# Performance work log

Hardware: AMD Instinct MI355X
Metric: run time of the kernel (lower is better)

Reference implementation:

```python
import jax, jax.numpy as jnp
from jax import lax
import numpy as np

# Mamba mixer dims (mamba-1.4b scale)
D_MODEL, D_INNER, D_STATE, D_CONV, DT_RANK = 2048, 4096, 16, 4, 128
B, L = 2, 1024


def setup_inputs() -> dict:
    key = jax.random.key(0)
    ks = jax.random.split(key, 10)
    s = 0.02
    x = jax.random.normal(ks[0], (B, L, D_MODEL), jnp.float32)
    W_in = jax.random.normal(ks[1], (2 * D_INNER, D_MODEL), jnp.float32) * s
    conv_w = jax.random.normal(ks[2], (D_INNER, D_CONV), jnp.float32) * s  # depthwise kernel
    conv_b = jax.random.normal(ks[3], (D_INNER,), jnp.float32) * s
    W_x = jax.random.normal(ks[4], (DT_RANK + 2 * D_STATE, D_INNER), jnp.float32) * s
    W_dt = jax.random.normal(ks[5], (D_INNER, DT_RANK), jnp.float32) * s
    b_dt = jax.random.normal(ks[6], (D_INNER,), jnp.float32) * s
    # S4D-real init: A = -[1..d_state] per channel
    A_log = jnp.log(jnp.broadcast_to(jnp.arange(1, D_STATE + 1, dtype=jnp.float32), (D_INNER, D_STATE)))
    Dp = jnp.ones((D_INNER,), jnp.float32)
    W_out = jax.random.normal(ks[7], (D_MODEL, D_INNER), jnp.float32) * s
    return {"x": x, "W_in": W_in, "conv_w": conv_w, "conv_b": conv_b,
            "W_x": W_x, "W_dt": W_dt, "b_dt": b_dt, "A_log": A_log,
            "Dp": Dp, "W_out": W_out}


def reference(x, W_in, conv_w, conv_b, W_x, W_dt, b_dt, A_log, Dp, W_out):
    b, l, _ = x.shape
    d_inner, d_state = A_log.shape
    dt_rank = W_dt.shape[1]
    d_conv = conv_w.shape[1]

    # in_proj -> x branch and gate z   [b,l,2*d_inner]
    xz = jnp.einsum('bld,ed->ble', x, W_in)
    xp, z = jnp.split(xz, 2, axis=-1)

    # causal depthwise conv1d (kernel size d_conv) + SiLU
    xpad = jnp.pad(xp, ((0, 0), (d_conv - 1, 0), (0, 0)))
    xc = conv_b + sum(xpad[:, k:k + l, :] * conv_w[:, k] for k in range(d_conv))
    xc = jax.nn.silu(xc)

    # input-dependent dt, B, C
    dbc = jnp.einsum('ble,fe->blf', xc, W_x)
    dt = dbc[..., :dt_rank]
    Bm = dbc[..., dt_rank:dt_rank + d_state]          # [b,l,s]
    Cm = dbc[..., dt_rank + d_state:]                 # [b,l,s]
    delta = jax.nn.softplus(jnp.einsum('blr,er->ble', dt, W_dt) + b_dt)  # [b,l,e]

    A = -jnp.exp(A_log)                               # [e,s]
    dA = jnp.exp(delta[..., None] * A)                # [b,l,e,s]
    dBx = delta[..., None] * Bm[:, :, None, :] * xc[..., None]  # [b,l,e,s]

    def step(h, inp):
        dA_t, dBx_t = inp                             # [b,e,s]
        h = dA_t * h + dBx_t
        return h, h

    h0 = jnp.zeros((b, d_inner, d_state), x.dtype)
    _, hs = lax.scan(step, h0, (jnp.swapaxes(dA, 0, 1), jnp.swapaxes(dBx, 0, 1)))
    hs = jnp.swapaxes(hs, 0, 1)                       # [b,l,e,s]

    y = jnp.einsum('bles,bls->ble', hs, Cm) + xc * Dp
    y = y * jax.nn.silu(z)
    return jnp.einsum('ble,de->bld', y, W_out)
```

## Files before the change

### kernel.cpp

```cpp
#include <hip/hip_runtime.h>
#include <cstdint>


typedef __bf16 bf16x8 __attribute__((ext_vector_type(8)));
typedef float f32x4 __attribute__((ext_vector_type(4)));

__device__ __forceinline__ unsigned short f2bf(float f) {
  uint32_t u = __float_as_uint(f);
  u += 0x7FFFu + ((u >> 16) & 1u);
  return (unsigned short)(u >> 16);
}

__device__ __forceinline__ float bf2f(unsigned short v) {
  return __uint_as_float(((uint32_t)v) << 16);
}

__device__ __forceinline__ float silu_f(float v) {
  return v / (1.f + __expf(-v));
}

__device__ __forceinline__ float softplus_f(float v) {
  return (v > 20.f) ? v : log1pf(__expf(v));
}

__global__ void cast_all(const float* __restrict__ x, const float* __restrict__ W_in,
                         const float* __restrict__ W_out, const float* __restrict__ W_dt,
                         const float* __restrict__ W_x,
                         unsigned short* __restrict__ x_bf, unsigned short* __restrict__ Win_bf,
                         unsigned short* __restrict__ Wout_bf, unsigned short* __restrict__ Wdt_bf,
                         unsigned short* __restrict__ Wx_bf) {
  int i = blockIdx.x * 256 + threadIdx.x;
  const float4* s4; ushort4* d4; int j;
  if (i < 1048576)      { s4 = (const float4*)x;     d4 = (ushort4*)x_bf;    j = i; }
  else if (i < 5242880) { s4 = (const float4*)W_in;  d4 = (ushort4*)Win_bf;  j = i - 1048576; }
  else if (i < 7340032) { s4 = (const float4*)W_out; d4 = (ushort4*)Wout_bf; j = i - 5242880; }
  else if (i < 7471104) { s4 = (const float4*)W_dt;  d4 = (ushort4*)Wdt_bf;  j = i - 7340032; }
  else {
    j = i - 7471104;
    ushort4 o = {0, 0, 0, 0};
    if (j < 163840) {
      float4 v = ((const float4*)W_x)[j];
      o.x = f2bf(v.x); o.y = f2bf(v.y); o.z = f2bf(v.z); o.w = f2bf(v.w);
    }
    ((ushort4*)Wx_bf)[j] = o;
    return;
  }
  float4 v = s4[j];
  ushort4 o; o.x = f2bf(v.x); o.y = f2bf(v.y); o.z = f2bf(v.z); o.w = f2bf(v.w);
  d4[j] = o;
}

#define BM 128
#define BN 128
#define BKK 32

__device__ __forceinline__ void stage_tile(const unsigned short* __restrict__ G,
                                           int ldK, int g0, int k0,
                                           unsigned short* lds, int wave, int lane) {
#pragma unroll
  for (int c = 0; c < 2; ++c) {
    int row = c * 64 + wave * 16 + (lane >> 2);
    int col = (lane & 3) * 8;
    const unsigned short* src = G + (size_t)(g0 + row) * ldK + (k0 + col);
    unsigned short* dst = lds + c * 2048 + wave * 512;
    __builtin_amdgcn_global_load_lds((__attribute__((address_space(1))) void*)(src),
                                     (__attribute__((address_space(3))) void*)(dst),
                                     16, 0, 0);
  }
}

__global__ __launch_bounds__(256)
void gemm_bt(const unsigned short* __restrict__ A, const unsigned short* __restrict__ B,
             float* __restrict__ C, int M, int N, int ldK, int kchunk,
             const float* __restrict__ bias_sp) {
  __shared__ unsigned short As[BM * BKK];
  __shared__ unsigned short Bs[BN * BKK];
  const int tid = threadIdx.x;
  const int wave = tid >> 6, lane = tid & 63;
  const int wr = wave >> 1, wc = wave & 1;
  const int m0 = blockIdx.y * BM, n0 = blockIdx.x * BN;
  const int lr = lane & 15, lg = lane >> 4;
  const int kb = blockIdx.z * kchunk, ke = kb + kchunk;
  C += (size_t)blockIdx.z * M * N;

  f32x4 zero = {0.f, 0.f, 0.f, 0.f};
  f32x4 acc[4][4];
#pragma unroll
  for (int i = 0; i < 4; ++i)
#pragma unroll
    for (int j = 0; j < 4; ++j) acc[i][j] = zero;

  for (int k0 = kb; k0 < ke; k0 += BKK) {
    stage_tile(A, ldK, m0, k0, As, wave, lane);
    stage_tile(B, ldK, n0, k0, Bs, wave, lane);
    __syncthreads();
    bf16x8 af[4], bfr[4];
#pragma unroll
    for (int i = 0; i < 4; ++i)
      af[i] = *reinterpret_cast<const bf16x8*>(&As[(wr * 64 + i * 16 + lr) * BKK + lg * 8]);
#pragma unroll
    for (int j = 0; j < 4; ++j)
      bfr[j] = *reinterpret_cast<const bf16x8*>(&Bs[(wc * 64 + j * 16 + lr) * BKK + lg * 8]);
#pragma unroll
    for (int i = 0; i < 4; ++i)
#pragma unroll
      for (int j = 0; j < 4; ++j)
        acc[i][j] = __builtin_amdgcn_mfma_f32_16x16x32_bf16(af[i], bfr[j], acc[i][j], 0, 0, 0);
    __syncthreads();
  }

#pragma unroll
  for (int i = 0; i < 4; ++i) {
#pragma unroll
    for (int j = 0; j < 4; ++j) {
      int mrow = m0 + wr * 64 + i * 16 + lg * 4;
      int ncol = n0 + wc * 64 + j * 16 + lr;
      if (bias_sp) {
        float bv = bias_sp[ncol];
#pragma unroll
        for (int r = 0; r < 4; ++r)
          C[(size_t)(mrow + r) * N + ncol] = softplus_f(acc[i][j][r] + bv);
      } else {
#pragma unroll
        for (int r = 0; r < 4; ++r)
          C[(size_t)(mrow + r) * N + ncol] = acc[i][j][r];
      }
    }
  }
}

__global__ void reduce8_dbc(const float* __restrict__ p, float* __restrict__ dbc,
                            unsigned short* __restrict__ dt_bf) {
  int i = blockIdx.x * 256 + threadIdx.x;
  float s = 0.f;
#pragma unroll
  for (int c = 0; c < 8; ++c) s += p[(size_t)c * 524288 + i];
  dbc[i] = s;
  int col = i & 255;
  if (col < 128) dt_bf[(size_t)(i >> 8) * 128 + col] = f2bf(s);
}

__global__ void reduce4_out(const float* __restrict__ p, float* __restrict__ out) {
  int i = blockIdx.x * 256 + threadIdx.x;
  const float4* p4 = reinterpret_cast<const float4*>(p);
  float4 a = p4[i], b = p4[i + 1048576], c = p4[i + 2097152], d = p4[i + 3145728];
  float4 r;
  r.x = (a.x + b.x) + (c.x + d.x); r.y = (a.y + b.y) + (c.y + d.y);
  r.z = (a.z + b.z) + (c.z + d.z); r.w = (a.w + b.w) + (c.w + d.w);
  reinterpret_cast<float4*>(out)[i] = r;
}

__global__ __launch_bounds__(512, 2)
void gemm_bt_8ph(const unsigned short* __restrict__ A,
                 const unsigned short* __restrict__ B,
                 float* __restrict__ C, int M, int N, int K, int nbm, int kchunk) {
  __shared__ unsigned short As[2][16384];
  __shared__ unsigned short Bs[2][16384];
  const int tid = threadIdx.x;
  const int wid = tid >> 6, lane = tid & 63;
  const int wr = wid >> 2, wc = wid & 3;
  const int lr = lane & 15, lg = lane >> 4;

  const int cpx = gridDim.x >> 3;
  const int x = blockIdx.x;
  const int wg = (x & 7) * cpx + (x >> 3);
  const int bm = wg % nbm, bn = wg / nbm;
  const int m0 = bm * 256, n0 = bn * 256;
  const int kb = blockIdx.z * kchunk;
  C += (size_t)blockIdx.z * M * N;

  f32x4 acc[8][4];
  f32x4 zero = {0.f, 0.f, 0.f, 0.f};
#pragma unroll
  for (int i = 0; i < 8; ++i)
#pragma unroll
    for (int j = 0; j < 4; ++j) acc[i][j] = zero;

  const int nt = kchunk / 64;

  auto QUANT = [&](int t, int q) {
    const int buf = t & 1;
    const int ks = q >> 1;
    const unsigned short* G = (q & 1) ? B : A;
    const int g0 = (q & 1) ? n0 : m0;
    unsigned short* lds = ((q & 1) ? &Bs[buf][0] : &As[buf][0]) + ks * 8192;
    const int k0 = kb + t * 64 + ks * 32;
#pragma unroll
    for (int r = 0; r < 2; ++r) {
      int row = r * 128 + (tid >> 2);
      int scol = ((tid & 3) * 8) ^ (((row >> 1) & 3) << 3);
      const unsigned short* src = G + (size_t)(g0 + row) * K + (k0 + scol);
      __builtin_amdgcn_global_load_lds(
          (__attribute__((address_space(1))) const void*)(src),
          (__attribute__((address_space(3))) void*)(lds + r * 4096 + tid * 8),
          16, 0, 0);
    }
  };

  auto RD_A = [&](int buf, int ks, int mf) -> bf16x8 {
    int row = wr * 128 + mf * 16 + lr;
    int col = (lg * 8) ^ (((row >> 1) & 3) << 3);
    return *reinterpret_cast<const bf16x8*>(&As[buf][ks * 8192 + row * 32 + col]);
  };
  auto RD_B = [&](int buf, int ks, int nf) -> bf16x8 {
    int row = wc * 64 + nf * 16 + lr;
    int col = (lg * 8) ^ (((row >> 1) & 3) << 3);
    return *reinterpret_cast<const bf16x8*>(&Bs[buf][ks * 8192 + row * 32 + col]);
  };

  QUANT(0, 0); QUANT(0, 1); QUANT(0, 2); QUANT(0, 3);
  asm volatile("s_waitcnt vmcnt(4)" ::: "memory");
  __builtin_amdgcn_s_barrier();

  bf16x8 a[8], b[4];
  for (int t = 0; t < nt; ++t) {
    const int buf = t & 1;
    const bool pf = (t + 1 < nt);
#pragma unroll
    for (int mf = 0; mf < 8; ++mf) a[mf] = RD_A(buf, 0, mf);
    b[0] = RD_B(buf, 0, 0); b[1] = RD_B(buf, 0, 1);
    if (pf) {
      QUANT(t + 1, 0);
      asm volatile("s_waitcnt vmcnt(6)" ::: "memory");
    } else {
      asm volatile("s_waitcnt vmcnt(4)" ::: "memory");
    }
    __builtin_amdgcn_s_barrier();
    asm volatile("s_waitcnt lgkmcnt(0)" ::: "memory");
    __builtin_amdgcn_sched_barrier(0);
    __builtin_amdgcn_s_setprio(1);
#pragma unroll
    for (int nf = 0; nf < 2; ++nf)
#pragma unroll
      for (int mf = 0; mf < 8; ++mf)
        acc[mf][nf] = __builtin_amdgcn_mfma_f32_16x16x32_bf16(a[mf], b[nf], acc[mf][nf], 0, 0, 0);
    __builtin_amdgcn_s_setprio(0);
    __builtin_amdgcn_s_barrier();
    b[2] = RD_B(buf, 0, 2); b[3] = RD_B(buf, 0, 3);
    if (pf) {
      QUANT(t + 1, 1);
      asm volatile("s_waitcnt vmcnt(4)" ::: "memory");
    } else {
      asm volatile("s_waitcnt vmcnt(0)" ::: "memory");
    }
    __builtin_amdgcn_s_barrier();
    asm volatile("s_waitcnt lgkmcnt(0)" ::: "memory");
    __builtin_amdgcn_sched_barrier(0);
    __builtin_amdgcn_s_setprio(1);
#pragma unroll
    for (int nf = 2; nf < 4; ++nf)
#pragma unroll
      for (int mf = 0; mf < 8; ++mf)
        acc[mf][nf] = __builtin_amdgcn_mfma_f32_16x16x32_bf16(a[mf], b[nf], acc[mf][nf], 0, 0, 0);
    __builtin_amdgcn_s_setprio(0);
    __builtin_amdgcn_s_barrier();
#pragma unroll
    for (int mf = 0; mf < 8; ++mf) a[mf] = RD_A(buf, 1, mf);
    b[0] = RD_B(buf, 1, 0); b[1] = RD_B(buf, 1, 1);
    if (pf) QUANT(t + 1, 2);
    __builtin_amdgcn_s_barrier();
    asm volatile("s_waitcnt lgkmcnt(0)" ::: "memory");
    __builtin_amdgcn_sched_barrier(0);
    __builtin_amdgcn_s_setprio(1);
#pragma unroll
    for (int nf = 0; nf < 2; ++nf)
#pragma unroll
      for (int mf = 0; mf < 8; ++mf)
        acc[mf][nf] = __builtin_amdgcn_mfma_f32_16x16x32_bf16(a[mf], b[nf], acc[mf][nf], 0, 0, 0);
    __builtin_amdgcn_s_setprio(0);
    __builtin_amdgcn_s_barrier();
    b[2] = RD_B(buf, 1, 2); b[3] = RD_B(buf, 1, 3);
    if (pf) {
      QUANT(t + 1, 3);
      asm volatile("s_waitcnt vmcnt(4)" ::: "memory");
    }
    __builtin_amdgcn_s_barrier();
    asm volatile("s_waitcnt lgkmcnt(0)" ::: "memory");
    __builtin_amdgcn_sched_barrier(0);
    __builtin_amdgcn_s_setprio(1);
#pragma unroll
    for (int nf = 2; nf < 4; ++nf)
#pragma unroll
      for (int mf = 0; mf < 8; ++mf)
        acc[mf][nf] = __builtin_amdgcn_mfma_f32_16x16x32_bf16(a[mf], b[nf], acc[mf][nf], 0, 0, 0);
    __builtin_amdgcn_s_setprio(0);
    __builtin_amdgcn_s_barrier();
  }

#pragma unroll
  for (int mf = 0; mf < 8; ++mf) {
#pragma unroll
    for (int nf = 0; nf < 4; ++nf) {
      int mrow = m0 + wr * 128 + mf * 16 + lg * 4;
      int ncol = n0 + wc * 64 + nf * 16 + lr;
#pragma unroll
      for (int r = 0; r < 4; ++r)
        C[(size_t)(mrow + r) * N + ncol] = acc[mf][nf][r];
    }
  }
}

__global__ void conv_silu_kernel(const float* __restrict__ xz,
                                 const float* __restrict__ conv_w,
                                 const float* __restrict__ conv_b,
                                 unsigned short* __restrict__ xc_bf) {
  int i4 = blockIdx.x * 256 + threadIdx.x;
  int e4 = i4 & 1023;
  int m = i4 >> 10;
  int l = m & 1023;
  float4 cw0 = reinterpret_cast<const float4*>(conv_w)[e4 * 4 + 0];
  float4 cw1 = reinterpret_cast<const float4*>(conv_w)[e4 * 4 + 1];
  float4 cw2 = reinterpret_cast<const float4*>(conv_w)[e4 * 4 + 2];
  float4 cw3 = reinterpret_cast<const float4*>(conv_w)[e4 * 4 + 3];
  float4 acc = reinterpret_cast<const float4*>(conv_b)[e4];
#pragma unroll
  for (int k = 0; k < 4; ++k) {
    if (l - 3 + k >= 0) {
      float4 xv = reinterpret_cast<const float4*>(xz)[(size_t)(m - 3 + k) * 2048 + e4];
      acc.x = fmaf(xv.x, ((const float*)&cw0)[k], acc.x);
      acc.y = fmaf(xv.y, ((const float*)&cw1)[k], acc.y);
      acc.z = fmaf(xv.z, ((const float*)&cw2)[k], acc.z);
      acc.w = fmaf(xv.w, ((const float*)&cw3)[k], acc.w);
    }
  }
  ushort4 o;
  o.x = f2bf(silu_f(acc.x)); o.y = f2bf(silu_f(acc.y));
  o.z = f2bf(silu_f(acc.z)); o.w = f2bf(silu_f(acc.w));
  reinterpret_cast<ushort4*>(xc_bf)[i4] = o;
}

__global__ __launch_bounds__(256)
void scan_pass1(const float* __restrict__ delta, const float* __restrict__ dbc,
                const unsigned short* __restrict__ xcb, const float* __restrict__ A_log,
                float* __restrict__ hfin, float* __restrict__ Pprod) {
  __shared__ float Bsh[1024];
  const int tid = threadIdx.x;
  const int bc = blockIdx.x >> 4;
  const int eg = blockIdx.x & 15;
  const int b = bc >> 4, c = bc & 15;
  const int e = eg * 256 + tid;
  const int mb = b * 1024 + c * 64;
  for (int i = tid; i < 1024; i += 256)
    Bsh[i] = dbc[(size_t)(mb + (i >> 4)) * 256 + 128 + (i & 15)];
  __syncthreads();

  float A[16];
  const float4* al = reinterpret_cast<const float4*>(A_log + (size_t)e * 16);
#pragma unroll
  for (int q = 0; q < 4; ++q) {
    float4 v = al[q];
    A[q * 4 + 0] = -__expf(v.x); A[q * 4 + 1] = -__expf(v.y);
    A[q * 4 + 2] = -__expf(v.z); A[q * 4 + 3] = -__expf(v.w);
  }
  float h[16], P[16];
#pragma unroll
  for (int s = 0; s < 16; ++s) { h[s] = 0.f; P[s] = 1.f; }

  for (int ll = 0; ll < 64; ++ll) {
    const size_t m = (size_t)(mb + ll);
    float dl = delta[m * 4096 + e];
    float dxc = dl * bf2f(xcb[m * 4096 + e]);
#pragma unroll
    for (int s = 0; s < 16; ++s) {
      float dA = __expf(dl * A[s]);
      P[s] *= dA;
      h[s] = fmaf(dA, h[s], Bsh[ll * 16 + s] * dxc);
    }
  }
  float* hp = hfin + ((size_t)bc * 4096 + e) * 16;
  float* pp = Pprod + ((size_t)bc * 4096 + e) * 16;
#pragma unroll
  for (int s = 0; s < 16; ++s) { hp[s] = h[s]; pp[s] = P[s]; }
}

__global__ void scan_pass2(float* __restrict__ hfin, const float* __restrict__ Pprod) {
  int idx = blockIdx.x * 256 + threadIdx.x;
  int b = idx >> 16;
  int es = idx & 65535;
  float H = 0.f;
  for (int c = 0; c < 16; ++c) {
    size_t o = ((size_t)(b * 16 + c) << 16) + es;
    float hf = hfin[o];
    float Pp = Pprod[o];
    hfin[o] = H;
    H = fmaf(Pp, H, hf);
  }
}

__global__ __launch_bounds__(256)
void scan_pass3(const float* __restrict__ delta, const float* __restrict__ dbc,
                const unsigned short* __restrict__ xcb, const float* __restrict__ xz,
                const float* __restrict__ A_log, const float* __restrict__ Dp,
                const float* __restrict__ hcarry, unsigned short* __restrict__ y_bf) {
  __shared__ float Bsh[1024];
  __shared__ float Csh[1024];
  const int tid = threadIdx.x;
  const int bc = blockIdx.x >> 4;
  const int eg = blockIdx.x & 15;
  const int b = bc >> 4, c = bc & 15;
  const int e = eg * 256 + tid;
  const int mb = b * 1024 + c * 64;
  for (int i = tid; i < 1024; i += 256) {
    size_t base = (size_t)(mb + (i >> 4)) * 256 + (i & 15);
    Bsh[i] = dbc[base + 128];
    Csh[i] = dbc[base + 144];
  }
  __syncthreads();

  float A[16];
  const float4* al = reinterpret_cast<const float4*>(A_log + (size_t)e * 16);
#pragma unroll
  for (int q = 0; q < 4; ++q) {
    float4 v = al[q];
    A[q * 4 + 0] = -__expf(v.x); A[q * 4 + 1] = -__expf(v.y);
    A[q * 4 + 2] = -__expf(v.z); A[q * 4 + 3] = -__expf(v.w);
  }
  float h[16];
  const float* hp = hcarry + ((size_t)bc * 4096 + e) * 16;
#pragma unroll
  for (int s = 0; s < 16; ++s) h[s] = hp[s];
  const float Dv = Dp[e];

  for (int ll = 0; ll < 64; ++ll) {
    const size_t m = (size_t)(mb + ll);
    float dl = delta[m * 4096 + e];
    float xcv = bf2f(xcb[m * 4096 + e]);
    float dxc = dl * xcv;
    float y = 0.f;
#pragma unroll
    for (int s = 0; s < 16; ++s) {
      float dA = __expf(dl * A[s]);
      h[s] = fmaf(dA, h[s], Bsh[ll * 16 + s] * dxc);
      y = fmaf(h[s], Csh[ll * 16 + s], y);
    }
    float z = xz[m * 8192 + 4096 + e];
    y = (y + xcv * Dv) * silu_f(z);
    y_bf[m * 4096 + e] = f2bf(y);
  }
}

extern "C" void kernel_launch(void* const* d_in, const int* in_sizes, int n_in,
                              void* d_out, int out_size, void* d_ws, size_t ws_size,
                              hipStream_t stream) {
  const float* x      = (const float*)d_in[0];
  const float* W_in   = (const float*)d_in[1];
  const float* conv_w = (const float*)d_in[2];
  const float* conv_b = (const float*)d_in[3];
  const float* W_x    = (const float*)d_in[4];
  const float* W_dt   = (const float*)d_in[5];
  const float* b_dt   = (const float*)d_in[6];
  const float* A_log  = (const float*)d_in[7];
  const float* Dp     = (const float*)d_in[8];
  const float* W_out  = (const float*)d_in[9];
  float* out = (float*)d_out;
  char* ws = (char*)d_ws;

  unsigned short* Win_bf    = (unsigned short*)(ws + 0);
  float*          gpart2    = (float*)(ws + 0);
  float*          delta     = (float*)(ws + 0);
  unsigned short* x_bf      = (unsigned short*)(ws + 33554432);
  unsigned short* y_bf      = (unsigned short*)(ws + 33554432);
  unsigned short* Wout_bf   = (unsigned short*)(ws + 50331648);
  unsigned short* Wx_bf     = (unsigned short*)(ws + 67108864);
  unsigned short* Wdt_bf    = (unsigned short*)(ws + 69206016);
  float*          xz        = (float*)(ws + 70254592);
  float*          gpart4    = (float*)(ws + 70254592);
  unsigned short* xc_bf     = (unsigned short*)(ws + 170917888);
  float*          hfin      = (float*)(ws + 137363456);
  float*          Pprod     = (float*)(ws + 145752064);
  float*          dbc       = (float*)(ws + 187695104);
  unsigned short* dt_bf     = (unsigned short*)(ws + 189792256);

  cast_all<<<30208, 256, 0, stream>>>(x, W_in, W_out, W_dt, W_x,
                                      x_bf, Win_bf, Wout_bf, Wdt_bf, Wx_bf);

  gemm_bt_8ph<<<256, 512, 0, stream>>>(x_bf, Win_bf, xz, 2048, 8192, 2048, 8, 2048);

  conv_silu_kernel<<<8192, 256, 0, stream>>>(xz, conv_w, conv_b, xc_bf);

  gemm_bt<<<dim3(2, 16, 8), 256, 0, stream>>>(xc_bf, Wx_bf, gpart2, 2048, 256, 4096, 512, nullptr);
  reduce8_dbc<<<2048, 256, 0, stream>>>(gpart2, dbc, dt_bf);

  gemm_bt<<<dim3(32, 16, 1), 256, 0, stream>>>(dt_bf, Wdt_bf, delta, 2048, 4096, 128, 128, b_dt);

  scan_pass1<<<512, 256, 0, stream>>>(delta, dbc, xc_bf, A_log, hfin, Pprod);
  scan_pass2<<<512, 256, 0, stream>>>(hfin, Pprod);
  scan_pass3<<<512, 256, 0, stream>>>(delta, dbc, xc_bf, xz, A_log, Dp, hfin, y_bf);

  gemm_bt_8ph<<<dim3(64, 1, 4), 512, 0, stream>>>(y_bf, Wout_bf, gpart4, 2048, 2048, 4096, 8, 1024);
  reduce4_out<<<4096, 256, 0, stream>>>(gpart4, out);
}
```

Baseline: 350.1 us.

## Store in-proj output as bf16 and compute dA via powers of exp(-delta)

The in-projection GEMM now writes xz in bf16 instead of fp32, so the conv and scan_pass3 kernels read half the bytes, and the workspace buffers are rearranged to match. The scan kernels check at runtime whether A equals -(s+1) for every state. When it does, they compute a single exp(-delta) and build all 16 dA values as its integer powers, replacing 16 exponentials per step with multiplies, and otherwise fall back to the general path. The fast path depends on the S4D-real initialisation of A_log in the test inputs, but it is guarded, so other inputs stay correct, and storing xz in bf16 adds rounding error.

```diff
diff --git a/kernel.cpp b/kernel.cpp
--- a/kernel.cpp
+++ b/kernel.cpp
@@ -150,10 +150,11 @@
   reinterpret_cast<float4*>(out)[i] = r;
 }
 
+template <typename OT>
 __global__ __launch_bounds__(512, 2)
 void gemm_bt_8ph(const unsigned short* __restrict__ A,
                  const unsigned short* __restrict__ B,
-                 float* __restrict__ C, int M, int N, int K, int nbm, int kchunk) {
+                 OT* __restrict__ C, int M, int N, int K, int nbm, int kchunk) {
   __shared__ unsigned short As[2][16384];
   __shared__ unsigned short Bs[2][16384];
   const int tid = threadIdx.x;
@@ -294,13 +295,17 @@
       int mrow = m0 + wr * 128 + mf * 16 + lg * 4;
       int ncol = n0 + wc * 64 + nf * 16 + lr;
 #pragma unroll
-      for (int r = 0; r < 4; ++r)
-        C[(size_t)(mrow + r) * N + ncol] = acc[mf][nf][r];
-    }
-  }
-}
-
-__global__ void conv_silu_kernel(const float* __restrict__ xz,
+      for (int r = 0; r < 4; ++r) {
+        if constexpr (sizeof(OT) == 2)
+          C[(size_t)(mrow + r) * N + ncol] = (OT)f2bf(acc[mf][nf][r]);
+        else
+          C[(size_t)(mrow + r) * N + ncol] = (OT)acc[mf][nf][r];
+      }
+    }
+  }
+}
+
+__global__ void conv_silu_kernel(const unsigned short* __restrict__ xzb,
                                  const float* __restrict__ conv_w,
                                  const float* __restrict__ conv_b,
                                  unsigned short* __restrict__ xc_bf) {
@@ -316,17 +321,25 @@
 #pragma unroll
   for (int k = 0; k < 4; ++k) {
     if (l - 3 + k >= 0) {
-      float4 xv = reinterpret_cast<const float4*>(xz)[(size_t)(m - 3 + k) * 2048 + e4];
-      acc.x = fmaf(xv.x, ((const float*)&cw0)[k], acc.x);
-      acc.y = fmaf(xv.y, ((const float*)&cw1)[k], acc.y);
-      acc.z = fmaf(xv.z, ((const float*)&cw2)[k], acc.z);
-      acc.w = fmaf(xv.w, ((const float*)&cw3)[k], acc.w);
+      ushort4 xv = reinterpret_cast<const ushort4*>(xzb)[(size_t)(m - 3 + k) * 2048 + e4];
+      acc.x = fmaf(bf2f(xv.x), ((const float*)&cw0)[k], acc.x);
+      acc.y = fmaf(bf2f(xv.y), ((const float*)&cw1)[k], acc.y);
+      acc.z = fmaf(bf2f(xv.z), ((const float*)&cw2)[k], acc.z);
+      acc.w = fmaf(bf2f(xv.w), ((const float*)&cw3)[k], acc.w);
     }
   }
   ushort4 o;
   o.x = f2bf(silu_f(acc.x)); o.y = f2bf(silu_f(acc.y));
   o.z = f2bf(silu_f(acc.z)); o.w = f2bf(silu_f(acc.w));
   reinterpret_cast<ushort4*>(xc_bf)[i4] = o;
+}
+
+__device__ __forceinline__ void dA_powers(float r, float* dA) {
+  float r2 = r * r, r4 = r2 * r2, r8 = r4 * r4;
+  dA[0] = r;        dA[1] = r2;       dA[2] = r2 * r;   dA[3] = r4;
+  dA[4] = r4 * r;   dA[5] = r4 * r2;  dA[6] = dA[5] * r; dA[7] = r8;
+  dA[8] = r8 * r;   dA[9] = r8 * r2;  dA[10] = dA[9] * r; dA[11] = r8 * r4;
+  dA[12] = dA[11] * r; dA[13] = dA[11] * r2; dA[14] = dA[13] * r; dA[15] = r8 * r8;
 }
 
 __global__ __launch_bounds__(256)
@@ -352,19 +365,39 @@
     A[q * 4 + 0] = -__expf(v.x); A[q * 4 + 1] = -__expf(v.y);
     A[q * 4 + 2] = -__expf(v.z); A[q * 4 + 3] = -__expf(v.w);
   }
+  bool fastp = true;
+#pragma unroll
+  for (int s = 0; s < 16; ++s)
+    fastp = fastp && (fabsf(A[s] + (float)(s + 1)) <= 1e-5f * (float)(s + 1));
+
   float h[16], P[16];
 #pragma unroll
   for (int s = 0; s < 16; ++s) { h[s] = 0.f; P[s] = 1.f; }
 
-  for (int ll = 0; ll < 64; ++ll) {
-    const size_t m = (size_t)(mb + ll);
-    float dl = delta[m * 4096 + e];
-    float dxc = dl * bf2f(xcb[m * 4096 + e]);
-#pragma unroll
-    for (int s = 0; s < 16; ++s) {
-      float dA = __expf(dl * A[s]);
-      P[s] *= dA;
-      h[s] = fmaf(dA, h[s], Bsh[ll * 16 + s] * dxc);
+  if (fastp) {
+    for (int ll = 0; ll < 64; ++ll) {
+      const size_t m = (size_t)(mb + ll);
+      float dl = delta[m * 4096 + e];
+      float dxc = dl * bf2f(xcb[m * 4096 + e]);
+      float dA[16];
+      dA_powers(__expf(-dl), dA);
+#pragma unroll
+      for (int s = 0; s < 16; ++s) {
+        P[s] *= dA[s];
+        h[s] = fmaf(dA[s], h[s], Bsh[ll * 16 + s] * dxc);
+      }
+    }
+  } else {
+    for (int ll = 0; ll < 64; ++ll) {
+      const size_t m = (size_t)(mb + ll);
+      float dl = delta[m * 4096 + e];
+      float dxc = dl * bf2f(xcb[m * 4096 + e]);
+#pragma unroll
+      for (int s = 0; s < 16; ++s) {
+        float dA = __expf(dl * A[s]);
+        P[s] *= dA;
+        h[s] = fmaf(dA, h[s], Bsh[ll * 16 + s] * dxc);
+      }
     }
   }
   float* hp = hfin + ((size_t)bc * 4096 + e) * 16;
@@ -389,7 +422,7 @@
 
 __global__ __launch_bounds__(256)
 void scan_pass3(const float* __restrict__ delta, const float* __restrict__ dbc,
-                const unsigned short* __restrict__ xcb, const float* __restrict__ xz,
+                const unsigned short* __restrict__ xcb, const unsigned short* __restrict__ xzb,
                 const float* __restrict__ A_log, const float* __restrict__ Dp,
                 const float* __restrict__ hcarry, unsigned short* __restrict__ y_bf) {
   __shared__ float Bsh[1024];
@@ -415,27 +448,52 @@
     A[q * 4 + 0] = -__expf(v.x); A[q * 4 + 1] = -__expf(v.y);
     A[q * 4 + 2] = -__expf(v.z); A[q * 4 + 3] = -__expf(v.w);
   }
+  bool fastp = true;
+#pragma unroll
+  for (int s = 0; s < 16; ++s)
+    fastp = fastp && (fabsf(A[s] + (float)(s + 1)) <= 1e-5f * (float)(s + 1));
+
   float h[16];
   const float* hp = hcarry + ((size_t)bc * 4096 + e) * 16;
 #pragma unroll
   for (int s = 0; s < 16; ++s) h[s] = hp[s];
   const float Dv = Dp[e];
 
-  for (int ll = 0; ll < 64; ++ll) {
-    const size_t m = (size_t)(mb + ll);
-    float dl = delta[m * 4096 + e];
-    float xcv = bf2f(xcb[m * 4096 + e]);
-    float dxc = dl * xcv;
-    float y = 0.f;
-#pragma unroll
-    for (int s = 0; s < 16; ++s) {
-      float dA = __expf(dl * A[s]);
-      h[s] = fmaf(dA, h[s], Bsh[ll * 16 + s] * dxc);
-      y = fmaf(h[s], Csh[ll * 16 + s], y);
-    }
-    float z = xz[m * 8192 + 4096 + e];
-    y = (y + xcv * Dv) * silu_f(z);
-    y_bf[m * 4096 + e] = f2bf(y);
+  if (fastp) {
+    for (int ll = 0; ll < 64; ++ll) {
+      const size_t m = (size_t)(mb + ll);
+      float dl = delta[m * 4096 + e];
+      float xcv = bf2f(xcb[m * 4096 + e]);
+      float dxc = dl * xcv;
+      float dA[16];
+      dA_powers(__expf(-dl), dA);
+      float y = 0.f;
+#pragma unroll
+      for (int s = 0; s < 16; ++s) {
+        h[s] = fmaf(dA[s], h[s], Bsh[ll * 16 + s] * dxc);
+        y = fmaf(h[s], Csh[ll * 16 + s], y);
+      }
+      float z = bf2f(xzb[m * 8192 + 4096 + e]);
+      y = (y + xcv * Dv) * silu_f(z);
+      y_bf[m * 4096 + e] = f2bf(y);
+    }
+  } else {
+    for (int ll = 0; ll < 64; ++ll) {
+      const size_t m = (size_t)(mb + ll);
+      float dl = delta[m * 4096 + e];
+      float xcv = bf2f(xcb[m * 4096 + e]);
+      float dxc = dl * xcv;
+      float y = 0.f;
+#pragma unroll
+      for (int s = 0; s < 16; ++s) {
+        float dA = __expf(dl * A[s]);
+        h[s] = fmaf(dA, h[s], Bsh[ll * 16 + s] * dxc);
+        y = fmaf(h[s], Csh[ll * 16 + s], y);
+      }
+      float z = bf2f(xzb[m * 8192 + 4096 + e]);
+      y = (y + xcv * Dv) * silu_f(z);
+      y_bf[m * 4096 + e] = f2bf(y);
+    }
   }
 }
 
@@ -463,20 +521,20 @@
   unsigned short* Wout_bf   = (unsigned short*)(ws + 50331648);
   unsigned short* Wx_bf     = (unsigned short*)(ws + 67108864);
   unsigned short* Wdt_bf    = (unsigned short*)(ws + 69206016);
-  float*          xz        = (float*)(ws + 70254592);
-  float*          gpart4    = (float*)(ws + 70254592);
+  unsigned short* xz_bf     = (unsigned short*)(ws + 70254592);
+  float*          gpart4    = (float*)(ws + 103809024);
+  float*          hfin      = (float*)(ws + 103809024);
+  float*          Pprod     = (float*)(ws + 112197632);
   unsigned short* xc_bf     = (unsigned short*)(ws + 170917888);
-  float*          hfin      = (float*)(ws + 137363456);
-  float*          Pprod     = (float*)(ws + 145752064);
   float*          dbc       = (float*)(ws + 187695104);
   unsigned short* dt_bf     = (unsigned short*)(ws + 189792256);
 
   cast_all<<<30208, 256, 0, stream>>>(x, W_in, W_out, W_dt, W_x,
                                       x_bf, Win_bf, Wout_bf, Wdt_bf, Wx_bf);
 
-  gemm_bt_8ph<<<256, 512, 0, stream>>>(x_bf, Win_bf, xz, 2048, 8192, 2048, 8, 2048);
-
-  conv_silu_kernel<<<8192, 256, 0, stream>>>(xz, conv_w, conv_b, xc_bf);
+  gemm_bt_8ph<unsigned short><<<256, 512, 0, stream>>>(x_bf, Win_bf, xz_bf, 2048, 8192, 2048, 8, 2048);
+
+  conv_silu_kernel<<<8192, 256, 0, stream>>>(xz_bf, conv_w, conv_b, xc_bf);
 
   gemm_bt<<<dim3(2, 16, 8), 256, 0, stream>>>(xc_bf, Wx_bf, gpart2, 2048, 256, 4096, 512, nullptr);
   reduce8_dbc<<<2048, 256, 0, stream>>>(gpart2, dbc, dt_bf);
@@ -485,8 +543,8 @@
 
   scan_pass1<<<512, 256, 0, stream>>>(delta, dbc, xc_bf, A_log, hfin, Pprod);
   scan_pass2<<<512, 256, 0, stream>>>(hfin, Pprod);
-  scan_pass3<<<512, 256, 0, stream>>>(delta, dbc, xc_bf, xz, A_log, Dp, hfin, y_bf);
-
-  gemm_bt_8ph<<<dim3(64, 1, 4), 512, 0, stream>>>(y_bf, Wout_bf, gpart4, 2048, 2048, 4096, 8, 1024);
+  scan_pass3<<<512, 256, 0, stream>>>(delta, dbc, xc_bf, xz_bf, A_log, Dp, hfin, y_bf);
+
+  gemm_bt_8ph<float><<<dim3(64, 1, 4), 512, 0, stream>>>(y_bf, Wout_bf, gpart4, 2048, 2048, 4096, 8, 1024);
   reduce4_out<<<4096, 256, 0, stream>>>(gpart4, out);
 }
```

Result: faster. 330.1 us (-5.7%).
